# Kernel optimization log

Measured on AMD Instinct MI355X. Metric: run time of the kernel, lower is better.

The kernel has to match this reference:

```python
import jax, jax.numpy as jnp
import numpy as np

HEADS = 16
DV = 64  # value_out_channel
DK = 64  # key_out_channel == query_out_channel
DQ = 64  # query_out_channel


def setup_inputs() -> dict:
    key = jax.random.key(0)
    ks = jax.random.split(key, 7)
    B, Skv, Ekv = 4, 2048, 1024
    Sq, Eq = 2048, 1024
    x = jax.random.normal(ks[0], (B, Skv, Ekv), dtype=jnp.float32)
    y = jax.random.normal(ks[1], (B, Sq, Eq), dtype=jnp.float32)
    # Linear weights stored as [in, out] for x @ W; no bias on qkv (bias=False)
    Wv = jax.random.normal(ks[2], (Ekv, HEADS * DV), dtype=jnp.float32) * (Ekv ** -0.5)
    Wk = jax.random.normal(ks[3], (Ekv, HEADS * DK), dtype=jnp.float32) * (Ekv ** -0.5)
    Wq = jax.random.normal(ks[4], (Eq, HEADS * DQ), dtype=jnp.float32) * (Eq ** -0.5)
    Wu = jax.random.normal(ks[5], (HEADS * DV, DQ), dtype=jnp.float32) * ((HEADS * DV) ** -0.5)
    bu = jax.random.normal(ks[6], (DQ,), dtype=jnp.float32) * 0.01
    return {"x": x, "y": y, "Wv": Wv, "Wk": Wk, "Wq": Wq, "Wu": Wu, "bu": bu}


def reference(x, y, Wv, Wk, Wq, Wu, bu):
    B, Skv, Ekv = x.shape
    _, Sq, Eq = y.shape
    v = (x @ Wv).reshape(B, Skv, HEADS, DV)
    k = (x @ Wk).reshape(B, Skv, HEADS, DK)
    q = (y @ Wq).reshape(B, Sq, HEADS, DQ)
    # scaling uses INPUT embedding dims, as in the source
    q = q * (Eq ** -0.25)
    k = k * (Ekv ** -0.25)
    dot = jnp.einsum("bqhd,bkhd->bhqk", q, k)  # [B, H, Sq, Skv]
    attn = jax.nn.softmax(dot, axis=-1)
    out = jnp.einsum("bhqk,bkhd->bqhd", attn, v).reshape(B, Sq, HEADS * DV)
    return out @ Wu + bu
```

## Files before the change

### kernel.cpp

```cpp
#include <hip/hip_runtime.h>
#include <hip/hip_bf16.h>
#include <stdint.h>

typedef short s16x8 __attribute__((ext_vector_type(8)));
typedef float f32x4 __attribute__((ext_vector_type(4)));

#define MFMA16(a, b, c) __builtin_amdgcn_mfma_f32_16x16x32_bf16((a), (b), (c), 0, 0, 0)

__device__ __forceinline__ void gld16(const __bf16* g, __bf16* l) {
  __builtin_amdgcn_global_load_lds(
      (const __attribute__((address_space(1))) unsigned int*)g,
      (__attribute__((address_space(3))) unsigned int*)l, 16, 0, 0);
}

__device__ __forceinline__ float fast_exp2(float x) {
#if __has_builtin(__builtin_amdgcn_exp2f)
  return __builtin_amdgcn_exp2f(x);
#else
  float r;
  asm("v_exp_f32 %0, %1" : "=v"(r) : "v"(x));
  return r;
#endif
}

__device__ __forceinline__ int probe_cnt_wave(const unsigned short* xs, int lane) {
  int cnt = 0;
  for (int i = lane; i < 1024; i += 64) {
    unsigned bits = ((unsigned)xs[2 * i]) << 16;
    float f = __uint_as_float(bits);
    float a = fabsf(f);
    if (f == f && a >= 1e-4f && a <= 1e4f) cnt++;
  }
#pragma unroll
  for (int off = 32; off; off >>= 1) cnt += __shfl_down(cnt, off);
  return cnt;
}

__global__ void probe_kernel(const unsigned short* __restrict__ x, int* __restrict__ flag) {
  int cnt = probe_cnt_wave(x, threadIdx.x & 63);
  if (threadIdx.x == 0) *flag = (cnt >= 512) ? 1 : 0;
}

__global__ void __launch_bounds__(256)
pre_kernel(const void* __restrict__ x, const void* __restrict__ y,
           const void* __restrict__ w0, const void* __restrict__ w1,
           const void* __restrict__ w2, const void* __restrict__ w3,
           __bf16* __restrict__ xb, __bf16* __restrict__ yb,
           __bf16* __restrict__ wqkvT, __bf16* __restrict__ wuT) {
  __shared__ int sflag;
  __shared__ float tile[32][33];
  if (threadIdx.x < 64) {
    int cnt = probe_cnt_wave((const unsigned short*)x, threadIdx.x);
    if (threadIdx.x == 0) sflag = (cnt >= 512) ? 1 : 0;
  }
  __syncthreads();
  const bool isbf = (sflag != 0);

  const int bid = blockIdx.x;
  if (bid < 2048) {
    constexpr int NV = (int)((size_t)8192 * 1024 / 8);
    int i = bid * 256 + threadIdx.x;
    const int stride = 2048 * 256;
    for (; i < 2 * NV; i += stride) {
      int v = (i < NV) ? i : i - NV;
      const void* in = (i < NV) ? x : y;
      __bf16* out = (i < NV) ? xb : yb;
      if (isbf) {
        *(uint4*)&out[v * 8] = *(const uint4*)&((const __bf16*)in)[v * 8];
      } else {
        float4 a = *(const float4*)&((const float*)in)[v * 8];
        float4 b = *(const float4*)&((const float*)in)[v * 8 + 4];
        union { __bf16 h[8]; uint4 u; } pk;
        pk.h[0] = (__bf16)a.x; pk.h[1] = (__bf16)a.y; pk.h[2] = (__bf16)a.z; pk.h[3] = (__bf16)a.w;
        pk.h[4] = (__bf16)b.x; pk.h[5] = (__bf16)b.y; pk.h[6] = (__bf16)b.z; pk.h[7] = (__bf16)b.w;
        *(uint4*)&out[v * 8] = pk.u;
      }
    }
  } else {
    int t = bid - 2048;
    int z, bx, by;
    if (t < 3072) { z = t >> 10; int xy = t & 1023; bx = xy & 31; by = xy >> 5; }
    else          { z = 3; int u = t - 3072; bx = u & 1; by = u >> 1; }
    const void* in = (z == 0) ? w0 : (z == 1) ? w1 : (z == 2) ? w2 : w3;
    __bf16* out = (z == 3) ? wuT : wqkvT + (size_t)z * 1024 * 1024;
    const int N = (z == 3) ? 64 : 1024;
    int tx = threadIdx.x & 31, ty = threadIdx.x >> 5;
    int n0 = bx * 32, k0 = by * 32;
#pragma unroll
    for (int i = 0; i < 32; i += 8) {
      size_t idx = (size_t)(k0 + ty + i) * N + (n0 + tx);
      tile[ty + i][tx] = isbf ? (float)((const __bf16*)in)[idx] : ((const float*)in)[idx];
    }
    __syncthreads();
#pragma unroll
    for (int i = 0; i < 32; i += 8)
      out[(size_t)(n0 + ty + i) * 1024 + (k0 + tx)] = (__bf16)tile[tx][ty + i];
  }
}

__global__ void tr3_kernel(const void* __restrict__ w0, const void* __restrict__ w1,
                           const void* __restrict__ w2, const void* __restrict__ w3,
                           __bf16* __restrict__ outbase, __bf16* __restrict__ out3,
                           const int* __restrict__ flag) {
  const bool isbf = (*flag != 0);
  const int z = blockIdx.z;
  if (z == 3 && blockIdx.x >= 2) return;
  const void* in = (z == 0) ? w0 : (z == 1) ? w1 : (z == 2) ? w2 : w3;
  __bf16* out = (z == 3) ? out3 : outbase + (size_t)z * 1024 * 1024;
  const int N = (z == 3) ? 64 : 1024;
  __shared__ float tile[32][33];
  int tx = threadIdx.x & 31, ty = threadIdx.x >> 5;
  int n0 = blockIdx.x * 32, k0 = blockIdx.y * 32;
#pragma unroll
  for (int i = 0; i < 32; i += 8) {
    size_t idx = (size_t)(k0 + ty + i) * N + (n0 + tx);
    tile[ty + i][tx] = isbf ? (float)((const __bf16*)in)[idx] : ((const float*)in)[idx];
  }
  __syncthreads();
#pragma unroll
  for (int i = 0; i < 32; i += 8)
    out[(size_t)(n0 + ty + i) * 1024 + (k0 + tx)] = (__bf16)tile[tx][ty + i];
}

__global__ void __launch_bounds__(256)
gemm_qkv(const __bf16* __restrict__ xb, const __bf16* __restrict__ yb,
         const __bf16* __restrict__ Wt,
         __bf16* __restrict__ qb, __bf16* __restrict__ kb, __bf16* __restrict__ vbT,
         float scq, float sck) {
  constexpr int BM = 128, BN = 128, BK = 32, K = 1024;
  __shared__ __attribute__((aligned(16))) __bf16 As[2][BM * BK];
  __shared__ __attribute__((aligned(16))) __bf16 Bs[2][BN * BK];

  const int tid = threadIdx.x;
  const int wid = tid >> 6, lane = tid & 63;
  const int quad = lane >> 4, l16 = lane & 15;
  const int wm = (wid >> 1) * 64, wn = (wid & 1) * 64;

  const int id = blockIdx.x;
  const int jj = id >> 3;
  const int ny = (id & 7) * 3 + (jj % 3);
  const int mb = jj / 3;
  const size_t m0 = (size_t)mb * BM;
  const size_t n0 = (size_t)ny * BN;
  const __bf16* A = (ny < 8) ? yb : xb;

  f32x4 acc[4][4];
#pragma unroll
  for (int i = 0; i < 4; ++i)
#pragma unroll
    for (int j = 0; j < 4; ++j) acc[i][j] = (f32x4){0.f, 0.f, 0.f, 0.f};

#pragma unroll
  for (int i = 0; i < 2; ++i) {
    int s = i * 256 + tid, r = s >> 2, c = (s & 3) * 8;
    gld16(&A[(m0 + r) * K + c], &As[0][(i * 256 + (tid & 192)) * 8]);
  }
#pragma unroll
  for (int i = 0; i < 2; ++i) {
    int s = i * 256 + tid, r = s >> 2, c = (s & 3) * 8;
    gld16(&Wt[(n0 + r) * K + c], &Bs[0][(i * 256 + (tid & 192)) * 8]);
  }

  for (int k0 = 0; k0 < K; k0 += BK) {
    const int cur = (k0 >> 5) & 1;
    asm volatile("s_waitcnt vmcnt(0)" ::: "memory");
    __builtin_amdgcn_s_barrier();
    asm volatile("" ::: "memory");

    if (k0 + BK < K) {
#pragma unroll
      for (int i = 0; i < 2; ++i) {
        int s = i * 256 + tid, r = s >> 2, c = (s & 3) * 8;
        gld16(&A[(m0 + r) * K + k0 + BK + c], &As[cur ^ 1][(i * 256 + (tid & 192)) * 8]);
      }
#pragma unroll
      for (int i = 0; i < 2; ++i) {
        int s = i * 256 + tid, r = s >> 2, c = (s & 3) * 8;
        gld16(&Wt[(n0 + r) * K + k0 + BK + c], &Bs[cur ^ 1][(i * 256 + (tid & 192)) * 8]);
      }
    }

    s16x8 af[4], bf[4];
#pragma unroll
    for (int mt = 0; mt < 4; ++mt)
      af[mt] = *(const s16x8*)&As[cur][(wm + mt * 16 + l16) * BK + quad * 8];
#pragma unroll
    for (int nt = 0; nt < 4; ++nt)
      bf[nt] = *(const s16x8*)&Bs[cur][(wn + nt * 16 + l16) * BK + quad * 8];
#pragma unroll
    for (int mt = 0; mt < 4; ++mt)
#pragma unroll
      for (int nt = 0; nt < 4; ++nt)
        acc[mt][nt] = MFMA16(af[mt], bf[nt], acc[mt][nt]);
  }

  if (ny < 16) {
    const float s = (ny < 8) ? scq : sck;
    __bf16* C = (ny < 8) ? qb : kb;
    const int nl0 = (ny < 8) ? (int)n0 : (int)n0 - 1024;
#pragma unroll
    for (int mt = 0; mt < 4; ++mt)
#pragma unroll
      for (int nt = 0; nt < 4; ++nt)
#pragma unroll
        for (int r = 0; r < 4; ++r) {
          size_t row = m0 + wm + mt * 16 + quad * 4 + r;
          size_t col = (size_t)(nl0 + wn + nt * 16 + l16);
          C[row * 1024 + col] = (__bf16)(acc[mt][nt][r] * s);
        }
  } else {
    __syncthreads();
    constexpr int LBS = 144;
    __bf16* bufA = As[0];
    __bf16* bufB = Bs[0];
    __bf16* mybuf = (wid & 1) ? bufB : bufA;
    const int colbase = (int)n0 - 2048;
    const int b = (int)(m0 >> 11);
    const int sq0 = (int)(m0 & 2047);
#pragma unroll
    for (int c = 0; c < 4; ++c) {
#pragma unroll
      for (int mt = 0; mt < 4; ++mt) {
        union { __bf16 h[4]; uint2 u; } pk;
#pragma unroll
        for (int r = 0; r < 4; ++r) pk.h[r] = (__bf16)acc[mt][c][r];
        *(uint2*)&mybuf[l16 * LBS + wm + mt * 16 + quad * 4] = pk.u;
      }
      __syncthreads();
      {
        const int p = tid >> 7;
        const __bf16* rb = p ? bufB : bufA;
        const int d16 = (tid >> 3) & 15;
        const int sc = tid & 7;
        const int colg = colbase + p * 64 + c * 16 + d16;
        const int hh = colg >> 6, dd = colg & 63;
        const size_t rowb = ((size_t)b * 16 + hh) * 64 + dd;
        uint4 v0 = *(const uint4*)&rb[d16 * LBS + sc * 16];
        uint4 v1 = *(const uint4*)&rb[d16 * LBS + sc * 16 + 8];
        *(uint4*)&vbT[rowb * 2048 + sq0 + sc * 16] = v0;
        *(uint4*)&vbT[rowb * 2048 + sq0 + sc * 16 + 8] = v1;
      }
      __syncthreads();
    }
  }
}

__global__ void __launch_bounds__(256)
gemm_out(const __bf16* __restrict__ A, const __bf16* __restrict__ Bt,
         void* __restrict__ Cv, const void* __restrict__ biasv,
         const unsigned short* __restrict__ xprobe) {
  constexpr int BK = 64, K = 1024, N = 64;
  __shared__ __attribute__((aligned(16))) __bf16 As[32 * BK];
  __shared__ __attribute__((aligned(16))) __bf16 Bs[64 * BK];
  __shared__ int sflag;

  const int tid = threadIdx.x;
  if (tid < 64) {
    int cnt = probe_cnt_wave(xprobe, tid);
    if (tid == 0) sflag = (cnt >= 512) ? 1 : 0;
  }

  const int wid = tid >> 6, lane = tid & 63;
  const int quad = lane >> 4, l16 = lane & 15;
  const int wm = (wid >> 1) * 16, wn = (wid & 1) * 32;
  const size_t m0 = (size_t)blockIdx.x * 32;

  f32x4 acc[2];
  acc[0] = (f32x4){0.f, 0.f, 0.f, 0.f};
  acc[1] = (f32x4){0.f, 0.f, 0.f, 0.f};

  for (int k0 = 0; k0 < K; k0 += BK) {
    {
      int r = tid >> 3, c = (tid & 7) * 8;
      gld16(&A[(m0 + r) * K + k0 + c], &As[(tid & 192) * 8]);
    }
#pragma unroll
    for (int i = 0; i < 2; ++i) {
      int s = i * 256 + tid, r = s >> 3, c = (s & 7) * 8;
      gld16(&Bt[r * K + k0 + c], &Bs[(i * 256 + (tid & 192)) * 8]);
    }
    __syncthreads();

#pragma unroll
    for (int kc = 0; kc < 2; ++kc) {
      s16x8 af = *(const s16x8*)&As[(wm + l16) * BK + kc * 32 + quad * 8];
#pragma unroll
      for (int nt = 0; nt < 2; ++nt) {
        s16x8 bf = *(const s16x8*)&Bs[(wn + nt * 16 + l16) * BK + kc * 32 + quad * 8];
        acc[nt] = MFMA16(af, bf, acc[nt]);
      }
    }
    __syncthreads();
  }

  const bool raw_bf = (sflag != 0);
#pragma unroll
  for (int nt = 0; nt < 2; ++nt)
#pragma unroll
    for (int r = 0; r < 4; ++r) {
      size_t row = m0 + wm + quad * 4 + r;
      size_t col = (size_t)(wn + nt * 16 + l16);
      float v = acc[nt][r];
      v += raw_bf ? (float)((const __bf16*)biasv)[col] : ((const float*)biasv)[col];
      if (raw_bf) ((__bf16*)Cv)[row * N + col] = (__bf16)v;
      else        ((float*)Cv)[row * N + col] = v;
    }
}

template <int BM, int BN, bool BIAS, bool A_WS, bool C_WS>
__global__ void __launch_bounds__(256)
gemm_bt(const void* __restrict__ Av, const __bf16* __restrict__ Bt,
        void* __restrict__ Cv, const void* __restrict__ biasv,
        int M, int N, int K, float scale, const int* __restrict__ flag) {
  constexpr int BK = 32;
  constexpr int LDT = BK + 8;
  __shared__ __attribute__((aligned(16))) __bf16 As[BM][LDT];
  __shared__ __attribute__((aligned(16))) __bf16 Bs[BN][LDT];
  constexpr int WM = BM / 2, WN = BN / 2;
  constexpr int MT = WM / 16, NT = WN / 16;

  const bool raw_bf = (*flag != 0);
  const bool a_bf = A_WS ? true : raw_bf;

  const int tid = threadIdx.x;
  const int wid = tid >> 6, lane = tid & 63;
  const int quad = lane >> 4, l16 = lane & 15;
  const int wm = (wid >> 1) * WM, wn = (wid & 1) * WN;
  const size_t m0 = (size_t)blockIdx.x * BM;
  const size_t n0 = (size_t)blockIdx.y * BN;

  f32x4 acc[MT][NT];
#pragma unroll
  for (int i = 0; i < MT; ++i)
#pragma unroll
    for (int j = 0; j < NT; ++j) acc[i][j] = (f32x4){0.f, 0.f, 0.f, 0.f};

  for (int k0 = 0; k0 < K; k0 += BK) {
    if (a_bf) {
      const __bf16* A = (const __bf16*)Av;
#pragma unroll
      for (int i = 0; i < (BM * 4) / 256; ++i) {
        int s = i * 256 + tid, r = s >> 2, c = (s & 3) * 8;
        *(uint4*)&As[r][c] = *(const uint4*)&A[(m0 + r) * K + k0 + c];
      }
    } else {
      const float* A = (const float*)Av;
#pragma unroll
      for (int i = 0; i < (BM * 8) / 256; ++i) {
        int s = i * 256 + tid, r = s >> 3, c = (s & 7) * 4;
        float4 t = *(const float4*)&A[(m0 + r) * K + k0 + c];
        union { __bf16 h[4]; uint2 u; } cv;
        cv.h[0] = (__bf16)t.x; cv.h[1] = (__bf16)t.y;
        cv.h[2] = (__bf16)t.z; cv.h[3] = (__bf16)t.w;
        *(uint2*)&As[r][c] = cv.u;
      }
    }
#pragma unroll
    for (int i = 0; i < (BN * 4) / 256; ++i) {
      int s = i * 256 + tid, r = s >> 2, c = (s & 3) * 8;
      *(uint4*)&Bs[r][c] = *(const uint4*)&Bt[(n0 + r) * K + k0 + c];
    }
    __syncthreads();

    s16x8 af[MT], bf[NT];
#pragma unroll
    for (int mt = 0; mt < MT; ++mt)
      af[mt] = *(const s16x8*)&As[wm + mt * 16 + l16][quad * 8];
#pragma unroll
    for (int nt = 0; nt < NT; ++nt)
      bf[nt] = *(const s16x8*)&Bs[wn + nt * 16 + l16][quad * 8];
#pragma unroll
    for (int mt = 0; mt < MT; ++mt)
#pragma unroll
      for (int nt = 0; nt < NT; ++nt)
        acc[mt][nt] = MFMA16(af[mt], bf[nt], acc[mt][nt]);
    __syncthreads();
  }

#pragma unroll
  for (int mt = 0; mt < MT; ++mt)
#pragma unroll
    for (int nt = 0; nt < NT; ++nt)
#pragma unroll
      for (int r = 0; r < 4; ++r) {
        size_t row = m0 + wm + mt * 16 + quad * 4 + r;
        size_t col = n0 + wn + nt * 16 + l16;
        float v = acc[mt][nt][r] * scale;
        if (BIAS)
          v += raw_bf ? (float)((const __bf16*)biasv)[col] : ((const float*)biasv)[col];
        if (C_WS || raw_bf) ((__bf16*)Cv)[row * N + col] = (__bf16)v;
        else                ((float*)Cv)[row * N + col] = v;
      }
}

__global__ void __launch_bounds__(256, 4)
attn5_kernel(const __bf16* __restrict__ qg, const __bf16* __restrict__ kg,
             const __bf16* __restrict__ vtg, __bf16* __restrict__ og) {
  constexpr int SKV = 2048, QT = 128, KT = 64, SS = 1024, VS = 2048;
  __shared__ __attribute__((aligned(16))) __bf16 QP[QT * 64];
  __shared__ __attribute__((aligned(16))) __bf16 Ks[KT * 64];
  __shared__ __attribute__((aligned(16))) __bf16 Vt[64 * KT];

  const int tid = threadIdx.x;
  const int wid = tid >> 6, lane = tid & 63;
  const int quad = lane >> 4, l16 = lane & 15;

  const int id = blockIdx.x;
  const int j = id >> 3;
  const int bh = (id & 7) * 8 + (j & 7);
  const int b = bh >> 4, h = bh & 15;
  const int q0 = (j >> 3) * QT;

  const __bf16* qb = qg + (size_t)b * 2048 * SS + h * 64;
  const __bf16* kb = kg + (size_t)b * 2048 * SS + h * 64;
  const __bf16* vtb = vtg + (size_t)bh * 64 * VS;
  __bf16* ob = og + (size_t)b * 2048 * SS + h * 64;

#pragma unroll
  for (int i = 0; i < 4; ++i) {
    int s = i * 256 + tid, r = s >> 3, slot = s & 7, c = slot ^ (r & 7);
    gld16(&qb[(size_t)(q0 + r) * SS + c * 8], &QP[(i * 256 + (tid & 192)) * 8]);
  }
  __syncthreads();

  s16x8 qf[2][2];
#pragma unroll
  for (int nt = 0; nt < 2; ++nt)
#pragma unroll
    for (int kc = 0; kc < 2; ++kc) {
      int row = wid * 32 + nt * 16 + l16;
      qf[nt][kc] = *(const s16x8*)&QP[row * 64 + (((quad + kc * 4) ^ (row & 7)) * 8)];
    }
  __syncthreads();

  int koff[4][2];
  int pwoff[2][4];
  int proff[2][2];
  int voff[2][4];
#pragma unroll
  for (int mtk = 0; mtk < 4; ++mtk)
#pragma unroll
    for (int kc = 0; kc < 2; ++kc) {
      int row = mtk * 16 + l16;
      koff[mtk][kc] = row * 64 + (((quad + kc * 4) ^ (row & 7)) * 8);
    }
#pragma unroll
  for (int ntq = 0; ntq < 2; ++ntq) {
    int row = wid * 32 + ntq * 16 + l16;
#pragma unroll
    for (int mtk = 0; mtk < 4; ++mtk)
      pwoff[ntq][mtk] = row * 64 + (((2 * mtk + (quad >> 1)) ^ (row & 7)) * 8) + (quad & 1) * 4;
#pragma unroll
    for (int kc = 0; kc < 2; ++kc)
      proff[ntq][kc] = row * 64 + (((4 * kc + quad) ^ (row & 7)) * 8);
  }
#pragma unroll
  for (int kc = 0; kc < 2; ++kc)
#pragma unroll
    for (int ntd = 0; ntd < 4; ++ntd) {
      int d = ntd * 16 + l16;
      voff[kc][ntd] = d * 64 + (((kc * 4 + quad) ^ (d & 7)) * 8);
    }

  float lsum[2] = {0.f, 0.f};
  f32x4 oacc[2][4];
#pragma unroll
  for (int mt = 0; mt < 2; ++mt)
#pragma unroll
    for (int nt = 0; nt < 4; ++nt) oacc[mt][nt] = (f32x4){0.f, 0.f, 0.f, 0.f};

#pragma unroll
  for (int i = 0; i < 2; ++i) {
    int s = i * 256 + tid, r = s >> 3, slot = s & 7, c = slot ^ (r & 7);
    gld16(&kb[(size_t)r * SS + c * 8], &Ks[(i * 256 + (tid & 192)) * 8]);
  }

  for (int kv = 0; kv < SKV; kv += KT) {
    asm volatile("s_waitcnt vmcnt(0)" ::: "memory");
    __builtin_amdgcn_s_barrier();

#pragma unroll
    for (int i = 0; i < 2; ++i) {
      int s = i * 256 + tid, r = s >> 3, slot = s & 7, c = slot ^ (r & 7);
      gld16(&vtb[(size_t)r * VS + kv + c * 8], &Vt[(i * 256 + (tid & 192)) * 8]);
    }

#pragma unroll
    for (int mtk = 0; mtk < 4; ++mtk) {
      s16x8 kfa[2];
#pragma unroll
      for (int kc = 0; kc < 2; ++kc)
        kfa[kc] = *(const s16x8*)&Ks[koff[mtk][kc]];
#pragma unroll
      for (int ntq = 0; ntq < 2; ++ntq) {
        f32x4 z = (f32x4){0.f, 0.f, 0.f, 0.f};
        __builtin_amdgcn_s_setprio(1);
        z = MFMA16(kfa[0], qf[ntq][0], z);
        z = MFMA16(kfa[1], qf[ntq][1], z);
        __builtin_amdgcn_s_setprio(0);
        union { __bf16 hh[4]; uint2 u; } pk;
        float p0 = fast_exp2(z[0]);
        float p1 = fast_exp2(z[1]);
        float p2 = fast_exp2(z[2]);
        float p3 = fast_exp2(z[3]);
        pk.hh[0] = (__bf16)p0; pk.hh[1] = (__bf16)p1;
        pk.hh[2] = (__bf16)p2; pk.hh[3] = (__bf16)p3;
        lsum[ntq] += (p0 + p1) + (p2 + p3);
        *(uint2*)&QP[pwoff[ntq][mtk]] = pk.u;
      }
    }

    asm volatile("s_waitcnt vmcnt(0)" ::: "memory");
    __builtin_amdgcn_s_barrier();

    if (kv + KT < SKV) {
#pragma unroll
      for (int i = 0; i < 2; ++i) {
        int s = i * 256 + tid, r = s >> 3, slot = s & 7, c = slot ^ (r & 7);
        gld16(&kb[(size_t)(kv + KT + r) * SS + c * 8], &Ks[(i * 256 + (tid & 192)) * 8]);
      }
    }

#pragma unroll
    for (int kc = 0; kc < 2; ++kc) {
      s16x8 pf[2], vf[4];
#pragma unroll
      for (int mt2 = 0; mt2 < 2; ++mt2)
        pf[mt2] = *(const s16x8*)&QP[proff[mt2][kc]];
#pragma unroll
      for (int ntd = 0; ntd < 4; ++ntd)
        vf[ntd] = *(const s16x8*)&Vt[voff[kc][ntd]];
      __builtin_amdgcn_s_setprio(1);
#pragma unroll
      for (int mt2 = 0; mt2 < 2; ++mt2)
#pragma unroll
        for (int ntd = 0; ntd < 4; ++ntd)
          oacc[mt2][ntd] = MFMA16(pf[mt2], vf[ntd], oacc[mt2][ntd]);
      __builtin_amdgcn_s_setprio(0);
    }
  }

#pragma unroll
  for (int nt = 0; nt < 2; ++nt) {
    lsum[nt] += __shfl_xor(lsum[nt], 16);
    lsum[nt] += __shfl_xor(lsum[nt], 32);
  }
#pragma unroll
  for (int mt2 = 0; mt2 < 2; ++mt2)
#pragma unroll
    for (int r = 0; r < 4; ++r) {
      float l = __shfl(lsum[mt2], quad * 4 + r);
      float linv = 1.0f / l;
      int row = q0 + wid * 32 + mt2 * 16 + quad * 4 + r;
#pragma unroll
      for (int ntd = 0; ntd < 4; ++ntd)
        ob[(size_t)row * SS + ntd * 16 + l16] = (__bf16)(oacc[mt2][ntd][r] * linv);
    }
}

__global__ void __launch_bounds__(256)
attn_kernel(const __bf16* __restrict__ qg, const __bf16* __restrict__ kg,
            const __bf16* __restrict__ vg, __bf16* __restrict__ og) {
  constexpr int D = 64, SKV = 2048, QT = 128, KT = 64, SS = 1024;
  constexpr int LDP = 72, LDV = 72;
  __shared__ __attribute__((aligned(16))) __bf16 QP[QT * LDP];
  __shared__ __attribute__((aligned(16))) __bf16 Ks[KT * D];
  __shared__ __attribute__((aligned(16))) __bf16 Vts[D * LDV];

  const int tid = threadIdx.x;
  const int wid = tid >> 6, lane = tid & 63;
  const int quad = lane >> 4, l16 = lane & 15;
  const int b = blockIdx.y >> 4, h = blockIdx.y & 15;
  const int q0 = blockIdx.x * QT;

  const __bf16* qb = qg + (size_t)b * 2048 * SS + h * D;
  const __bf16* kb = kg + (size_t)b * 2048 * SS + h * D;
  const __bf16* vb = vg + (size_t)b * 2048 * SS + h * D;
  __bf16* ob = og + (size_t)b * 2048 * SS + h * D;

#pragma unroll
  for (int i = 0; i < 4; ++i) {
    int s = i * 256 + tid, r = s >> 3, slot = s & 7, c = slot ^ (r & 7);
    gld16(&qb[(size_t)(q0 + r) * SS + c * 8], &QP[(i * 256 + (tid & 192)) * 8]);
  }
  __syncthreads();

  s16x8 qf[2][2];
#pragma unroll
  for (int nt = 0; nt < 2; ++nt)
#pragma unroll
    for (int kc = 0; kc < 2; ++kc) {
      int row = wid * 32 + nt * 16 + l16;
      qf[nt][kc] = *(const s16x8*)&QP[row * 64 + (((quad + kc * 4) ^ (row & 7)) * 8)];
    }
  __syncthreads();

  float lsum[2] = {0.f, 0.f};
  f32x4 oacc[2][4];
#pragma unroll
  for (int mt = 0; mt < 2; ++mt)
#pragma unroll
    for (int nt = 0; nt < 4; ++nt) oacc[mt][nt] = (f32x4){0.f, 0.f, 0.f, 0.f};

  for (int kv = 0; kv < SKV; kv += KT) {
#pragma unroll
    for (int i = 0; i < 2; ++i) {
      int s = i * 256 + tid, r = s >> 3, slot = s & 7, c = slot ^ (r & 7);
      gld16(&kb[(size_t)(kv + r) * SS + c * 8], &Ks[(i * 256 + (tid & 192)) * 8]);
    }
#pragma unroll
    for (int i = 0; i < 2; ++i) {
      int s = i * 256 + tid, r = s >> 3, mc = s & 7;
      uint4 t = *(const uint4*)&vb[(size_t)(kv + r) * SS + mc * 8];
      const __bf16* tp = (const __bf16*)&t;
      int colbase = r ^ (mc << 3);
#pragma unroll
      for (int jj = 0; jj < 8; ++jj) Vts[(mc * 8 + jj) * LDV + colbase] = tp[jj];
    }
    __syncthreads();

#pragma unroll
    for (int mtk = 0; mtk < 4; ++mtk) {
      s16x8 kfa[2];
#pragma unroll
      for (int kc = 0; kc < 2; ++kc) {
        int row = mtk * 16 + l16;
        kfa[kc] = *(const s16x8*)&Ks[row * 64 + (((quad + kc * 4) ^ (row & 7)) * 8)];
      }
#pragma unroll
      for (int ntq = 0; ntq < 2; ++ntq) {
        f32x4 z = (f32x4){0.f, 0.f, 0.f, 0.f};
        z = MFMA16(kfa[0], qf[ntq][0], z);
        z = MFMA16(kfa[1], qf[ntq][1], z);
        union { __bf16 hh[4]; uint2 u; } pk;
        float ps = 0.f;
#pragma unroll
        for (int r = 0; r < 4; ++r) {
          float p = __builtin_exp2f(fminf(z[r], 80.f));
          ps += p;
          pk.hh[r] = (__bf16)p;
        }
        lsum[ntq] += ps;
        int row = wid * 32 + ntq * 16 + l16;
        *(uint2*)&QP[row * LDP + mtk * 16 + quad * 4] = pk.u;
      }
    }

#pragma unroll
    for (int kc = 0; kc < 2; ++kc) {
      s16x8 pf[2], vf[4];
#pragma unroll
      for (int mt2 = 0; mt2 < 2; ++mt2)
        pf[mt2] = *(const s16x8*)&QP[(wid * 32 + mt2 * 16 + l16) * LDP + kc * 32 + quad * 8];
#pragma unroll
      for (int ntd = 0; ntd < 4; ++ntd) {
        int d = ntd * 16 + l16;
        int col0 = (kc * 32 + quad * 8) ^ ((((d >> 3) & 7)) << 3);
        vf[ntd] = *(const s16x8*)&Vts[d * LDV + col0];
      }
#pragma unroll
      for (int mt2 = 0; mt2 < 2; ++mt2)
#pragma unroll
        for (int ntd = 0; ntd < 4; ++ntd)
          oacc[mt2][ntd] = MFMA16(pf[mt2], vf[ntd], oacc[mt2][ntd]);
    }
    __syncthreads();
  }

#pragma unroll
  for (int nt = 0; nt < 2; ++nt) {
    lsum[nt] += __shfl_xor(lsum[nt], 16);
    lsum[nt] += __shfl_xor(lsum[nt], 32);
  }
#pragma unroll
  for (int mt2 = 0; mt2 < 2; ++mt2)
#pragma unroll
    for (int r = 0; r < 4; ++r) {
      float l = __shfl(lsum[mt2], quad * 4 + r);
      float linv = 1.0f / l;
      int row = q0 + wid * 32 + mt2 * 16 + quad * 4 + r;
#pragma unroll
      for (int ntd = 0; ntd < 4; ++ntd)
        ob[(size_t)row * SS + ntd * 16 + l16] = (__bf16)(oacc[mt2][ntd][r] * linv);
    }
}

extern "C" void kernel_launch(void* const* d_in, const int* in_sizes, int n_in,
                              void* d_out, int out_size, void* d_ws, size_t ws_size,
                              hipStream_t stream) {
  const void* x  = d_in[0];
  const void* y  = d_in[1];
  const void* Wv = d_in[2];
  const void* Wk = d_in[3];
  const void* Wq = d_in[4];
  const void* Wu = d_in[5];
  const void* bu = d_in[6];

  const float sc  = 0.17677669529663687f;
  const float scq = 0.17677669529663687f * 1.4426950408889634f;

  constexpr size_t NTOK = (size_t)8192 * 1024;
  constexpr size_t TB = NTOK * 2;

  char* p = (char*)d_ws;
  int* flag = (int*)p; p += 256;
  __bf16* qb = (__bf16*)p; p += TB;
  __bf16* kb = (__bf16*)p; p += TB;
  __bf16* vb = (__bf16*)p; p += TB;
  __bf16* WuT = (__bf16*)p; p += (size_t)64 * 1024 * 2;

  const size_t fast_need = 256 + 3 * TB + (size_t)64 * 1024 * 2 + 2 * TB + 3 * (size_t)1024 * 1024 * 2;
  if (ws_size >= fast_need) {
    __bf16* xb = (__bf16*)p; p += TB;
    __bf16* yb = (__bf16*)p; p += TB;
    __bf16* WqkvT = (__bf16*)p;
    __bf16* vbT = vb;
    __bf16* ob  = xb;

    pre_kernel<<<dim3(5184), 256, 0, stream>>>(x, y, Wq, Wk, Wv, Wu, xb, yb, WqkvT, WuT);

    gemm_qkv<<<dim3(1536), 256, 0, stream>>>(xb, yb, WqkvT, qb, kb, vbT, scq, sc);

    attn5_kernel<<<dim3(1024), 256, 0, stream>>>(qb, kb, vbT, ob);

    gemm_out<<<dim3(256), 256, 0, stream>>>(ob, WuT, d_out, bu, (const unsigned short*)x);
  } else {
    __bf16* region = (__bf16*)p;
    __bf16* WqT = region;
    __bf16* WkT = region + (size_t)1024 * 1024;
    __bf16* WvT = region + (size_t)2 * 1024 * 1024;
    __bf16* ob  = region;

    probe_kernel<<<1, 64, 0, stream>>>((const unsigned short*)x, flag);
    tr3_kernel<<<dim3(32, 32, 4), 256, 0, stream>>>(Wq, Wk, Wv, Wu, WqT, WuT, flag);

    gemm_bt<128, 128, false, false, true><<<dim3(64, 8), 256, 0, stream>>>(
        y, WqT, qb, nullptr, 8192, 1024, 1024, scq, flag);
    gemm_bt<128, 128, false, false, true><<<dim3(64, 8), 256, 0, stream>>>(
        x, WkT, kb, nullptr, 8192, 1024, 1024, sc, flag);
    gemm_bt<128, 128, false, false, true><<<dim3(64, 8), 256, 0, stream>>>(
        x, WvT, vb, nullptr, 8192, 1024, 1024, 1.0f, flag);

    attn_kernel<<<dim3(16, 64), 256, 0, stream>>>(qb, kb, vb, ob);

    gemm_bt<128, 64, true, true, false><<<dim3(64, 1), 256, 0, stream>>>(
        ob, WuT, d_out, bu, 8192, 64, 1024, 1.0f, flag);
  }
}
```

Before: 276.6 us.

## Fuse fp32-to-bf16 activation conversion into QKV GEMM tile loads

Removes the separate pass that converted x and y to bf16 in the pre-kernel. The QKV GEMM now reads fp32 activations directly, converts them in registers and stores bf16 into LDS, with the next tile's global loads issued before the MFMAs and written to LDS after them. This saves a full read/write round trip of the activations. In exchange, each activation tile is re-read as fp32 (twice the bytes) by every N-block that uses it, a per-block probe is added, and the async global-to-LDS path is replaced by register staging for the fp32 case.

After: 324.6 us. 17.4% more time.

```diff
diff --git a/kernel.cpp b/kernel.cpp
--- a/kernel.cpp
+++ b/kernel.cpp
@@ -42,10 +42,9 @@
 }
 
 __global__ void __launch_bounds__(256)
-pre_kernel(const void* __restrict__ x, const void* __restrict__ y,
+pre_kernel(const void* __restrict__ x,
            const void* __restrict__ w0, const void* __restrict__ w1,
            const void* __restrict__ w2, const void* __restrict__ w3,
-           __bf16* __restrict__ xb, __bf16* __restrict__ yb,
            __bf16* __restrict__ wqkvT, __bf16* __restrict__ wuT) {
   __shared__ int sflag;
   __shared__ float tile[32][33];
@@ -56,46 +55,24 @@
   __syncthreads();
   const bool isbf = (sflag != 0);
 
-  const int bid = blockIdx.x;
-  if (bid < 2048) {
-    constexpr int NV = (int)((size_t)8192 * 1024 / 8);
-    int i = bid * 256 + threadIdx.x;
-    const int stride = 2048 * 256;
-    for (; i < 2 * NV; i += stride) {
-      int v = (i < NV) ? i : i - NV;
-      const void* in = (i < NV) ? x : y;
-      __bf16* out = (i < NV) ? xb : yb;
-      if (isbf) {
-        *(uint4*)&out[v * 8] = *(const uint4*)&((const __bf16*)in)[v * 8];
-      } else {
-        float4 a = *(const float4*)&((const float*)in)[v * 8];
-        float4 b = *(const float4*)&((const float*)in)[v * 8 + 4];
-        union { __bf16 h[8]; uint4 u; } pk;
-        pk.h[0] = (__bf16)a.x; pk.h[1] = (__bf16)a.y; pk.h[2] = (__bf16)a.z; pk.h[3] = (__bf16)a.w;
-        pk.h[4] = (__bf16)b.x; pk.h[5] = (__bf16)b.y; pk.h[6] = (__bf16)b.z; pk.h[7] = (__bf16)b.w;
-        *(uint4*)&out[v * 8] = pk.u;
-      }
-    }
-  } else {
-    int t = bid - 2048;
-    int z, bx, by;
-    if (t < 3072) { z = t >> 10; int xy = t & 1023; bx = xy & 31; by = xy >> 5; }
-    else          { z = 3; int u = t - 3072; bx = u & 1; by = u >> 1; }
-    const void* in = (z == 0) ? w0 : (z == 1) ? w1 : (z == 2) ? w2 : w3;
-    __bf16* out = (z == 3) ? wuT : wqkvT + (size_t)z * 1024 * 1024;
-    const int N = (z == 3) ? 64 : 1024;
-    int tx = threadIdx.x & 31, ty = threadIdx.x >> 5;
-    int n0 = bx * 32, k0 = by * 32;
-#pragma unroll
-    for (int i = 0; i < 32; i += 8) {
-      size_t idx = (size_t)(k0 + ty + i) * N + (n0 + tx);
-      tile[ty + i][tx] = isbf ? (float)((const __bf16*)in)[idx] : ((const float*)in)[idx];
-    }
-    __syncthreads();
-#pragma unroll
-    for (int i = 0; i < 32; i += 8)
-      out[(size_t)(n0 + ty + i) * 1024 + (k0 + tx)] = (__bf16)tile[tx][ty + i];
-  }
+  const int t = blockIdx.x;
+  int z, bx, by;
+  if (t < 3072) { z = t >> 10; int xy = t & 1023; bx = xy & 31; by = xy >> 5; }
+  else          { z = 3; int u = t - 3072; bx = u & 1; by = u >> 1; }
+  const void* in = (z == 0) ? w0 : (z == 1) ? w1 : (z == 2) ? w2 : w3;
+  __bf16* out = (z == 3) ? wuT : wqkvT + (size_t)z * 1024 * 1024;
+  const int N = (z == 3) ? 64 : 1024;
+  int tx = threadIdx.x & 31, ty = threadIdx.x >> 5;
+  int n0 = bx * 32, k0 = by * 32;
+#pragma unroll
+  for (int i = 0; i < 32; i += 8) {
+    size_t idx = (size_t)(k0 + ty + i) * N + (n0 + tx);
+    tile[ty + i][tx] = isbf ? (float)((const __bf16*)in)[idx] : ((const float*)in)[idx];
+  }
+  __syncthreads();
+#pragma unroll
+  for (int i = 0; i < 32; i += 8)
+    out[(size_t)(n0 + ty + i) * 1024 + (k0 + tx)] = (__bf16)tile[tx][ty + i];
 }
 
 __global__ void tr3_kernel(const void* __restrict__ w0, const void* __restrict__ w1,
@@ -123,15 +100,23 @@
 }
 
 __global__ void __launch_bounds__(256)
-gemm_qkv(const __bf16* __restrict__ xb, const __bf16* __restrict__ yb,
+gemm_qkv(const void* __restrict__ xr, const void* __restrict__ yr,
          const __bf16* __restrict__ Wt,
          __bf16* __restrict__ qb, __bf16* __restrict__ kb, __bf16* __restrict__ vbT,
          float scq, float sck) {
   constexpr int BM = 128, BN = 128, BK = 32, K = 1024;
   __shared__ __attribute__((aligned(16))) __bf16 As[2][BM * BK];
   __shared__ __attribute__((aligned(16))) __bf16 Bs[2][BN * BK];
+  __shared__ int sflag;
 
   const int tid = threadIdx.x;
+  if (tid < 64) {
+    int cnt = probe_cnt_wave((const unsigned short*)xr, tid);
+    if (tid == 0) sflag = (cnt >= 512) ? 1 : 0;
+  }
+  __syncthreads();
+  const bool isbf = (sflag != 0);
+
   const int wid = tid >> 6, lane = tid & 63;
   const int quad = lane >> 4, l16 = lane & 15;
   const int wm = (wid >> 1) * 64, wn = (wid & 1) * 64;
@@ -142,7 +127,12 @@
   const int mb = jj / 3;
   const size_t m0 = (size_t)mb * BM;
   const size_t n0 = (size_t)ny * BN;
-  const __bf16* A = (ny < 8) ? yb : xb;
+  const void* Ar = (ny < 8) ? yr : xr;
+  const __bf16* Ab = (const __bf16*)Ar;
+  const float* Af = (const float*)Ar;
+
+  const int r0 = tid >> 2, c0 = (tid & 3) * 8;
+  const int r1 = (256 + tid) >> 2, c1 = c0;
 
   f32x4 acc[4][4];
 #pragma unroll
@@ -150,10 +140,23 @@
 #pragma unroll
     for (int j = 0; j < 4; ++j) acc[i][j] = (f32x4){0.f, 0.f, 0.f, 0.f};
 
-#pragma unroll
-  for (int i = 0; i < 2; ++i) {
-    int s = i * 256 + tid, r = s >> 2, c = (s & 3) * 8;
-    gld16(&A[(m0 + r) * K + c], &As[0][(i * 256 + (tid & 192)) * 8]);
+  if (isbf) {
+#pragma unroll
+    for (int i = 0; i < 2; ++i) {
+      int s = i * 256 + tid, r = s >> 2, c = (s & 3) * 8;
+      gld16(&Ab[(m0 + r) * K + c], &As[0][(i * 256 + (tid & 192)) * 8]);
+    }
+  } else {
+#pragma unroll
+    for (int i = 0; i < 2; ++i) {
+      int s = i * 256 + tid, r = s >> 2, c = (s & 3) * 8;
+      const float* ap = &Af[(m0 + r) * K + c];
+      float4 f0 = *(const float4*)ap, f1 = *(const float4*)(ap + 4);
+      union { __bf16 h[8]; uint4 u; } pk;
+      pk.h[0] = (__bf16)f0.x; pk.h[1] = (__bf16)f0.y; pk.h[2] = (__bf16)f0.z; pk.h[3] = (__bf16)f0.w;
+      pk.h[4] = (__bf16)f1.x; pk.h[5] = (__bf16)f1.y; pk.h[6] = (__bf16)f1.z; pk.h[7] = (__bf16)f1.w;
+      *(uint4*)&As[0][s * 8] = pk.u;
+    }
   }
 #pragma unroll
   for (int i = 0; i < 2; ++i) {
@@ -163,15 +166,24 @@
 
   for (int k0 = 0; k0 < K; k0 += BK) {
     const int cur = (k0 >> 5) & 1;
-    asm volatile("s_waitcnt vmcnt(0)" ::: "memory");
+    asm volatile("s_waitcnt vmcnt(0) lgkmcnt(0)" ::: "memory");
     __builtin_amdgcn_s_barrier();
     asm volatile("" ::: "memory");
 
-    if (k0 + BK < K) {
-#pragma unroll
-      for (int i = 0; i < 2; ++i) {
-        int s = i * 256 + tid, r = s >> 2, c = (s & 3) * 8;
-        gld16(&A[(m0 + r) * K + k0 + BK + c], &As[cur ^ 1][(i * 256 + (tid & 192)) * 8]);
+    const bool more = (k0 + BK < K);
+    float4 fa0, fa1, fb0, fb1;
+    if (more) {
+      if (isbf) {
+#pragma unroll
+        for (int i = 0; i < 2; ++i) {
+          int s = i * 256 + tid, r = s >> 2, c = (s & 3) * 8;
+          gld16(&Ab[(m0 + r) * K + k0 + BK + c], &As[cur ^ 1][(i * 256 + (tid & 192)) * 8]);
+        }
+      } else {
+        const float* ap0 = &Af[(m0 + r0) * K + k0 + BK + c0];
+        fa0 = *(const float4*)ap0; fa1 = *(const float4*)(ap0 + 4);
+        const float* ap1 = &Af[(m0 + r1) * K + k0 + BK + c1];
+        fb0 = *(const float4*)ap1; fb1 = *(const float4*)(ap1 + 4);
       }
 #pragma unroll
       for (int i = 0; i < 2; ++i) {
@@ -192,6 +204,16 @@
 #pragma unroll
       for (int nt = 0; nt < 4; ++nt)
         acc[mt][nt] = MFMA16(af[mt], bf[nt], acc[mt][nt]);
+
+    if (more && !isbf) {
+      union { __bf16 h[8]; uint4 u; } p0, p1;
+      p0.h[0] = (__bf16)fa0.x; p0.h[1] = (__bf16)fa0.y; p0.h[2] = (__bf16)fa0.z; p0.h[3] = (__bf16)fa0.w;
+      p0.h[4] = (__bf16)fa1.x; p0.h[5] = (__bf16)fa1.y; p0.h[6] = (__bf16)fa1.z; p0.h[7] = (__bf16)fa1.w;
+      *(uint4*)&As[cur ^ 1][tid * 8] = p0.u;
+      p1.h[0] = (__bf16)fb0.x; p1.h[1] = (__bf16)fb0.y; p1.h[2] = (__bf16)fb0.z; p1.h[3] = (__bf16)fb0.w;
+      p1.h[4] = (__bf16)fb1.x; p1.h[5] = (__bf16)fb1.y; p1.h[6] = (__bf16)fb1.z; p1.h[7] = (__bf16)fb1.w;
+      *(uint4*)&As[cur ^ 1][(256 + tid) * 8] = p1.u;
+    }
   }
 
   if (ny < 16) {
@@ -716,10 +738,11 @@
     __bf16* WqkvT = (__bf16*)p;
     __bf16* vbT = vb;
     __bf16* ob  = xb;
-
-    pre_kernel<<<dim3(5184), 256, 0, stream>>>(x, y, Wq, Wk, Wv, Wu, xb, yb, WqkvT, WuT);
-
-    gemm_qkv<<<dim3(1536), 256, 0, stream>>>(xb, yb, WqkvT, qb, kb, vbT, scq, sc);
+    (void)yb;
+
+    pre_kernel<<<dim3(3136), 256, 0, stream>>>(x, Wq, Wk, Wv, Wu, WqkvT, WuT);
+
+    gemm_qkv<<<dim3(1536), 256, 0, stream>>>(x, y, WqkvT, qb, kb, vbT, scq, sc);
 
     attn5_kernel<<<dim3(1024), 256, 0, stream>>>(qb, kb, vbT, ob);
 
```
